# Kernel optimization log

Measured on AMD Instinct MI355X. Metric: run time of the kernel, lower is better.

Reference implementation:

```python
import jax, jax.numpy as jnp
import numpy as np

TEXT_DIM = 1024
FEAT_DIM = 1024
NUM_HEADS = 16
HEAD_DIM = FEAT_DIM // NUM_HEADS
EPS = 1e-6


def rms_norm(x, w):
    # LlamaRMSNorm: compute in fp32, scale by learned weight
    xf = x.astype(jnp.float32)
    var = jnp.mean(xf * xf, axis=-1, keepdims=True)
    return (xf * jax.lax.rsqrt(var + EPS)).astype(x.dtype) * w


def setup_inputs() -> dict:
    key = jax.random.key(0)
    ks = jax.random.split(key, 8)
    def xavier(k, shape, gain=1.0):
        fan_in, fan_out = shape[1], shape[0]
        lim = gain * np.sqrt(6.0 / (fan_in + fan_out))
        return jax.random.uniform(k, shape, jnp.float32, -lim, lim)
    return {
        "text": jax.random.normal(ks[0], (8, 512, TEXT_DIM), jnp.float32),
        "features": jax.random.normal(ks[1], (8, 1024, FEAT_DIM), jnp.float32),
        "W_q": xavier(ks[2], (FEAT_DIM, TEXT_DIM)),
        "b_q": jnp.zeros((FEAT_DIM,), jnp.float32),
        "W_k": xavier(ks[3], (FEAT_DIM, FEAT_DIM)),
        "b_k": jnp.zeros((FEAT_DIM,), jnp.float32),
        "W_o": xavier(ks[4], (FEAT_DIM, FEAT_DIM), gain=0.1),
        "b_o": jnp.zeros((FEAT_DIM,), jnp.float32),
        "g_feat": jnp.ones((FEAT_DIM,), jnp.float32),
        "g_q": jnp.ones((FEAT_DIM,), jnp.float32),
        "g_k": jnp.ones((FEAT_DIM,), jnp.float32),
    }


def reference(text, features, W_q, b_q, W_k, b_k, W_o, b_o, g_feat, g_q, g_k):
    B, T, _ = text.shape
    _, N, _ = features.shape
    feats = rms_norm(features, g_feat)                      # [B,N,Df]
    Q = rms_norm(text @ W_q.T + b_q, g_q)                   # [B,T,Df]
    K = rms_norm(feats @ W_k.T + b_k, g_k)                  # [B,N,Df]
    Qh = Q.reshape(B, T, NUM_HEADS, HEAD_DIM)
    Kh = K.reshape(B, N, NUM_HEADS, HEAD_DIM)
    Vh = feats.reshape(B, N, NUM_HEADS, HEAD_DIM)
    scores = jnp.einsum("bthd,bnhd->bhtn", Qh, Kh) / np.sqrt(HEAD_DIM).astype(np.float32)
    attn = jax.nn.softmax(scores, axis=-1)                  # [B,H,T,N]
    out = jnp.einsum("bhtn,bnhd->bthd", attn, Vh).reshape(B, T, FEAT_DIM)
    return out @ W_o.T + b_o
```

## Files before the change

### kernel.cpp

```cpp
#include <hip/hip_runtime.h>
#include <hip/hip_bf16.h>


typedef unsigned short u16;
typedef __bf16 bf16x8 __attribute__((ext_vector_type(8)));
typedef float f32x4 __attribute__((ext_vector_type(4)));

__device__ inline f32x4 mfma16(bf16x8 a, bf16x8 b, f32x4 c) {
    return __builtin_amdgcn_mfma_f32_16x16x32_bf16(a, b, c, 0, 0, 0);
}

__device__ inline u16 f2bf(float f) {
    union { float f; unsigned u; } v; v.f = f;
    unsigned r = v.u + 0x7fffu + ((v.u >> 16) & 1u);
    return (u16)(r >> 16);
}

__device__ inline float bf2f(u16 x) {
    union { unsigned u; float f; } v; v.u = ((unsigned)x) << 16; return v.f;
}

__device__ inline unsigned pk_bf16(float a, float b) {
    union { float f; unsigned u; } x, y; x.f = a; y.f = b;
    return __builtin_amdgcn_perm(y.u + 0x8000u, x.u + 0x8000u, 0x07060302u);
}

__device__ inline void load_lds16(const void* g, void* l) {
    __builtin_amdgcn_global_load_lds(
        (const __attribute__((address_space(1))) void*)g,
        (__attribute__((address_space(3))) void*)l, 16, 0, 0);
}

__global__ __launch_bounds__(256) void cast_rows_kernel(const float* __restrict__ text,
                                                        const float* __restrict__ Wq,
                                                        const float* __restrict__ Wk,
                                                        const float* __restrict__ Wo,
                                                        const float* __restrict__ features,
                                                        u16* __restrict__ otext, u16* __restrict__ oWq,
                                                        u16* __restrict__ oWk, u16* __restrict__ oWo,
                                                        float* __restrict__ ssbuf) {
    int blk = blockIdx.x, tid = threadIdx.x;
    if (blk < 7168) {
        int i = blk * 256 + tid;
        const float* src; u16* dst; int off;
        if (i < 1048576)      { src = text; dst = otext; off = i; }
        else if (i < 1310720) { src = Wq;   dst = oWq;   off = i - 1048576; }
        else if (i < 1572864) { src = Wk;   dst = oWk;   off = i - 1310720; }
        else                  { src = Wo;   dst = oWo;   off = i - 1572864; }
        float4 v = ((const float4*)src)[off];
        uint2 p; p.x = pk_bf16(v.x, v.y); p.y = pk_bf16(v.z, v.w);
        ((uint2*)dst)[off] = p;
    } else {
        int row = (blk - 7168) * 4 + (tid >> 6);
        int lane = tid & 63;
        const float4* rp = (const float4*)(features + (size_t)row * 1024) + lane * 4;
        float ss = 0.0f;
        #pragma unroll
        for (int i = 0; i < 4; ++i) {
            float4 v = rp[i];
            ss += v.x * v.x + v.y * v.y + v.z * v.z + v.w * v.w;
        }
        #pragma unroll
        for (int m = 1; m < 64; m <<= 1) ss += __shfl_xor(ss, m, 64);
        if (lane == 0) ssbuf[row] = ss;
    }
}

__global__ __launch_bounds__(256) void normT_kernel(const float* __restrict__ features,
                                                    const float* __restrict__ ssbuf,
                                                    const float* __restrict__ g,
                                                    u16* __restrict__ feats_bf,
                                                    u16* __restrict__ Vt) {
    __shared__ __align__(16) u16 tile[64][72];
    int tid = threadIdx.x, b = blockIdx.z;
    int n0 = blockIdx.x * 64, d0 = blockIdx.y * 64;
    int r = tid >> 2, cs = (tid & 3) * 16;
    int grow = b * 1024 + n0 + r;

    float rs = rsqrtf(ssbuf[grow] * (1.0f / 1024.0f) + 1e-6f);
    const float4* src = (const float4*)(features + (size_t)grow * 1024 + d0 + cs);
    const float4* gp  = (const float4*)(g + d0 + cs);
    union { u16 s[16]; uint4 v[2]; } ob;
    #pragma unroll
    for (int i = 0; i < 4; ++i) {
        float4 v = src[i], gv = gp[i];
        unsigned lo = pk_bf16(v.x * rs * gv.x, v.y * rs * gv.y);
        unsigned hi = pk_bf16(v.z * rs * gv.z, v.w * rs * gv.w);
        ((unsigned*)ob.s)[i * 2]     = lo;
        ((unsigned*)ob.s)[i * 2 + 1] = hi;
    }
    uint4* dst = (uint4*)(feats_bf + (size_t)grow * 1024 + d0 + cs);
    dst[0] = ob.v[0]; dst[1] = ob.v[1];
    #pragma unroll
    for (int i = 0; i < 16; ++i) tile[r][cs + i] = ob.s[i];
    __syncthreads();
    union { u16 s[8]; uint4 v; } t0, t1;
    #pragma unroll
    for (int i = 0; i < 8; ++i) { t0.s[i] = tile[cs + i][r]; t1.s[i] = tile[cs + 8 + i][r]; }
    u16* tdst = Vt + ((size_t)(b * 1024 + d0 + r)) * 1024 + n0 + cs;
    *(uint4*)tdst = t0.v;
    *(uint4*)(tdst + 8) = t1.v;
}

__global__ __launch_bounds__(256) void rmsnorm_qk_kernel(u16* __restrict__ QK,
                                                         const float* __restrict__ g_q,
                                                         const float* __restrict__ g_k,
                                                         float qscale) {
    int tid = threadIdx.x;
    int row = blockIdx.x * 4 + (tid >> 6);
    int lane = tid & 63;
    const float* g = (row < 4096) ? g_q : g_k;
    float outsc = (row < 4096) ? qscale : 1.0f;

    u16* rp = QK + (size_t)row * 1024 + lane * 16;
    union { u16 s[16]; uint4 v[2]; } in;
    in.v[0] = *(const uint4*)rp;
    in.v[1] = *(const uint4*)(rp + 8);
    float x[16], ss = 0.0f;
    #pragma unroll
    for (int i = 0; i < 16; ++i) { x[i] = bf2f(in.s[i]); ss += x[i] * x[i]; }
    #pragma unroll
    for (int m = 1; m < 64; m <<= 1) ss += __shfl_xor(ss, m, 64);
    float rs = rsqrtf(ss * (1.0f / 1024.0f) + 1e-6f) * outsc;
    const float4* gp = (const float4*)(g + lane * 16);
    union { unsigned u[8]; uint4 v[2]; } ob;
    #pragma unroll
    for (int i = 0; i < 4; ++i) {
        float4 gv = gp[i];
        ob.u[i * 2]     = pk_bf16(x[i * 4 + 0] * rs * gv.x, x[i * 4 + 1] * rs * gv.y);
        ob.u[i * 2 + 1] = pk_bf16(x[i * 4 + 2] * rs * gv.z, x[i * 4 + 3] * rs * gv.w);
    }
    *(uint4*)rp = ob.v[0];
    *(uint4*)(rp + 8) = ob.v[1];
}

template <bool BF16OUT>
__device__ __forceinline__ void gemm64_bk64(const u16* __restrict__ A, const u16* __restrict__ B,
                                            const float* __restrict__ bias, void* __restrict__ Cout,
                                            int m_blk, int n_blk, int K, int N,
                                            u16* As, u16* Bs) {
    int tid = threadIdx.x, wave = tid >> 6, lane = tid & 63;
    int quad = lane >> 4, l15 = lane & 15;
    int wm = wave & 1, wn = wave >> 1;
    int srl = lane >> 3, scl = lane & 7;
    const int swz = (scl ^ srl) * 8;

    f32x4 acc[4][2] = {};

    auto stage = [&](int buf, int k0) {
        u16* Ad = As + buf * (128 * 64);
        u16* Bd = Bs + buf * (64 * 64);
        #pragma unroll
        for (int is = 0; is < 4; ++is) {
            int row = is * 32 + wave * 8 + srl;
            load_lds16(A + (size_t)(m_blk + row) * K + k0 + swz,
                       Ad + (is * 32 + wave * 8) * 64);
        }
        #pragma unroll
        for (int is = 0; is < 2; ++is) {
            int row = is * 32 + wave * 8 + srl;
            load_lds16(B + (size_t)(n_blk + row) * K + k0 + swz,
                       Bd + (is * 32 + wave * 8) * 64);
        }
    };

    stage(0, 0);
    __syncthreads();
    int cur = 0;

    for (int k0 = 0; k0 < K; k0 += 64) {
        if (k0 + 64 < K) stage(cur ^ 1, k0 + 64);

        const u16* Ar = As + cur * (128 * 64);
        const u16* Br = Bs + cur * (64 * 64);
        #pragma unroll
        for (int kh = 0; kh < 2; ++kh) {
            bf16x8 af[4], bfr[2];
            int co = ((kh * 4 + quad) ^ (l15 & 7)) * 8;
            #pragma unroll
            for (int t = 0; t < 4; ++t)
                af[t] = *(const bf16x8*)&Ar[(wm * 64 + t * 16 + l15) * 64 + co];
            #pragma unroll
            for (int t = 0; t < 2; ++t)
                bfr[t] = *(const bf16x8*)&Br[(wn * 32 + t * 16 + l15) * 64 + co];
            #pragma unroll
            for (int mt = 0; mt < 4; ++mt)
                #pragma unroll
                for (int nt = 0; nt < 2; ++nt)
                    acc[mt][nt] = mfma16(af[mt], bfr[nt], acc[mt][nt]);
        }
        __syncthreads();
        cur ^= 1;
    }

    #pragma unroll
    for (int nt = 0; nt < 2; ++nt) {
        int col = n_blk + wn * 32 + nt * 16 + l15;
        float bv = bias[col];
        #pragma unroll
        for (int mt = 0; mt < 4; ++mt) {
            int row0 = m_blk + wm * 64 + mt * 16 + quad * 4;
            #pragma unroll
            for (int r = 0; r < 4; ++r) {
                float val = acc[mt][nt][r] + bv;
                if (BF16OUT) ((u16*)Cout)[(size_t)(row0 + r) * N + col] = f2bf(val);
                else       ((float*)Cout)[(size_t)(row0 + r) * N + col] = val;
            }
        }
    }
}

__global__ __launch_bounds__(256) void gemm_qk_kernel(const u16* __restrict__ text_bf,
                                                      const u16* __restrict__ Wq,
                                                      const u16* __restrict__ feats_bf,
                                                      const u16* __restrict__ Wk,
                                                      const float* __restrict__ b_q,
                                                      const float* __restrict__ b_k,
                                                      u16* __restrict__ QK) {
    __shared__ __align__(16) u16 As[2 * 128 * 64];
    __shared__ __align__(16) u16 Bs[2 * 64 * 64];
    int id = blockIdx.x;
    if (id < 512) {
        gemm64_bk64<true>(text_bf, Wq, b_q, QK, (id & 31) * 128, (id >> 5) * 64, 1024, 1024, As, Bs);
    } else {
        id -= 512;
        gemm64_bk64<true>(feats_bf, Wk, b_k, QK + 4096 * 1024,
                          (id & 63) * 128, (id >> 6) * 64, 1024, 1024, As, Bs);
    }
}

__global__ __launch_bounds__(256) void gemm_o_kernel(const u16* __restrict__ A,
                                                     const u16* __restrict__ B,
                                                     const float* __restrict__ bias,
                                                     float* __restrict__ C) {
    __shared__ __align__(16) u16 As[2 * 128 * 64];
    __shared__ __align__(16) u16 Bs[2 * 64 * 64];
    int id = blockIdx.x;
    gemm64_bk64<false>(A, B, bias, C, (id & 31) * 128, (id >> 5) * 64, 1024, 1024, As, Bs);
}

__global__ __launch_bounds__(256) void attn_kernel(const u16* __restrict__ Q,
                                                   const u16* __restrict__ K,
                                                   const u16* __restrict__ Vt,
                                                   u16* __restrict__ Out) {
    int bh = blockIdx.x, qt = blockIdx.y;
    int b = bh >> 4, h = bh & 15;
    int tid = threadIdx.x, wave = tid >> 6, lane = tid & 63;
    int quad = lane >> 4, l15 = lane & 15;

    __shared__ __align__(16) u16 Ks[2][64 * 64];
    __shared__ __align__(16) u16 Vs[2][64 * 64];
    __shared__ __align__(16) u16 Plds[4][16 * 64];
    u16* Pw = &Plds[wave][0];
    const int psw = (l15 & 7) << 3;

    const size_t qoff = ((size_t)(b * 512 + qt * 64 + wave * 16 + l15)) * 1024 + h * 64 + quad * 8;
    bf16x8 qf0 = *(const bf16x8*)(Q + qoff);
    bf16x8 qf1 = *(const bf16x8*)(Q + qoff + 32);

    int srl = lane >> 3, scl = lane & 7;
    const u16* Kbase = K + ((size_t)(b * 1024)) * 1024 + h * 64;
    const u16* Vbase = Vt + ((size_t)(b * 1024 + h * 64)) * 1024;

    __bf16 onev = (__bf16)1.0f;
    bf16x8 ones = {onev, onev, onev, onev, onev, onev, onev, onev};

    f32x4 o[4] = {};
    f32x4 lac = {0.0f, 0.0f, 0.0f, 0.0f};

    auto stage = [&](int buf, int n0) {
        #pragma unroll
        for (int j = 0; j < 2; ++j) {
            int row = wave * 16 + j * 8 + srl;
            load_lds16(Kbase + (size_t)(n0 + row) * 1024 + (scl ^ srl) * 8,
                       &Ks[buf][(wave * 16 + j * 8) * 64]);
            load_lds16(Vbase + (size_t)row * 1024 + n0 + (scl ^ srl) * 8,
                       &Vs[buf][(wave * 16 + j * 8) * 64]);
        }
    };

    stage(0, 0);
    __syncthreads();
    int cur = 0;

    for (int n0 = 0; n0 < 1024; n0 += 64) {
        if (n0 < 960) stage(cur ^ 1, n0 + 64);

        f32x4 s[4];
        __builtin_amdgcn_s_setprio(1);
        #pragma unroll
        for (int nt = 0; nt < 4; ++nt) {
            int R = nt * 16 + l15;
            int c1 = (quad ^ (l15 & 7)) * 8;
            bf16x8 kf0 = *(const bf16x8*)&Ks[cur][R * 64 + c1];
            bf16x8 kf1 = *(const bf16x8*)&Ks[cur][R * 64 + (c1 ^ 32)];
            f32x4 z = {-16.0f, -16.0f, -16.0f, -16.0f};
            s[nt] = mfma16(kf0, qf0, z);
            s[nt] = mfma16(kf1, qf1, s[nt]);
        }
        __builtin_amdgcn_s_setprio(0);

        #pragma unroll
        for (int nt = 0; nt < 4; ++nt) {
            uint2 pk;
            pk.x = pk_bf16(exp2f(s[nt][0]), exp2f(s[nt][1]));
            pk.y = pk_bf16(exp2f(s[nt][2]), exp2f(s[nt][3]));
            *(uint2*)&Pw[l15 * 64 + ((nt * 16 + quad * 4) ^ psw)] = pk;
        }

        bf16x8 pf[2];
        #pragma unroll
        for (int kc = 0; kc < 2; ++kc)
            pf[kc] = *(const bf16x8*)&Pw[l15 * 64 + ((kc * 32 + quad * 8) ^ psw)];
        __builtin_amdgcn_s_setprio(1);
        #pragma unroll
        for (int kc = 0; kc < 2; ++kc) {
            lac = mfma16(ones, pf[kc], lac);
            #pragma unroll
            for (int dt = 0; dt < 4; ++dt) {
                int d = dt * 16 + l15;
                int ch = ((kc * 4 + quad) ^ (l15 & 7)) * 8;
                bf16x8 vf = *(const bf16x8*)&Vs[cur][d * 64 + ch];
                o[dt] = mfma16(vf, pf[kc], o[dt]);
            }
        }
        __builtin_amdgcn_s_setprio(0);

        __syncthreads();
        cur ^= 1;
    }

    float il = 1.0f / lac[0];
    size_t obase = ((size_t)(b * 512 + qt * 64 + wave * 16 + l15)) * 1024 + h * 64 + quad * 4;
    #pragma unroll
    for (int dt = 0; dt < 4; ++dt) {
        uint2 pk;
        pk.x = pk_bf16(o[dt][0] * il, o[dt][1] * il);
        pk.y = pk_bf16(o[dt][2] * il, o[dt][3] * il);
        *(uint2*)(Out + obase + dt * 16) = pk;
    }
}

extern "C" void kernel_launch(void* const* d_in, const int* in_sizes, int n_in,
                              void* d_out, int out_size, void* d_ws, size_t ws_size,
                              hipStream_t stream) {
    const float* text     = (const float*)d_in[0];
    const float* features = (const float*)d_in[1];
    const float* W_q      = (const float*)d_in[2];
    const float* b_q      = (const float*)d_in[3];
    const float* W_k      = (const float*)d_in[4];
    const float* b_k      = (const float*)d_in[5];
    const float* W_o      = (const float*)d_in[6];
    const float* b_o      = (const float*)d_in[7];
    const float* g_feat   = (const float*)d_in[8];
    const float* g_q      = (const float*)d_in[9];
    const float* g_k      = (const float*)d_in[10];

    char* ws = (char*)d_ws;
    u16*   text_bf  = (u16*)(ws + 0);
    u16*   Wq_bf    = (u16*)(ws + 8388608);
    u16*   Wk_bf    = (u16*)(ws + 10485760);
    u16*   Wo_bf    = (u16*)(ws + 12582912);
    u16*   feats_bf = (u16*)(ws + 14680064);
    u16*   Vt       = (u16*)(ws + 31457280);
    u16*   QKbuf    = (u16*)(ws + 48234496);
    u16*   attn_bf  = (u16*)(ws + 73400320);
    float* ssbuf    = (float*)(ws + 81788928);

    const float QSCALE = 0.18033688011112042f;

    cast_rows_kernel<<<9216, 256, 0, stream>>>(text, W_q, W_k, W_o, features,
                                               text_bf, Wq_bf, Wk_bf, Wo_bf, ssbuf);
    normT_kernel<<<dim3(16, 16, 8), 256, 0, stream>>>(features, ssbuf, g_feat, feats_bf, Vt);
    gemm_qk_kernel<<<1536, 256, 0, stream>>>(text_bf, Wq_bf, feats_bf, Wk_bf, b_q, b_k, QKbuf);
    rmsnorm_qk_kernel<<<3072, 256, 0, stream>>>(QKbuf, g_q, g_k, QSCALE);
    attn_kernel<<<dim3(128, 8), 256, 0, stream>>>(QKbuf, QKbuf + 4096 * 1024, Vt, attn_bf);
    gemm_o_kernel<<<512, 256, 0, stream>>>(attn_bf, Wo_bf, b_o, (float*)d_out);
}
```

Before: 225.2 us.

## Split attention waves 2x2 over query and key tiles with LDS reduction

Reorganizes the attention kernel so each wave handles 32 query rows and half of each 64-key tile, instead of 16 query rows and the full tile. This reuses each loaded K and V fragment across two query subtiles, cutting LDS reads per MFMA. Partial outputs and softmax denominators from the two key halves are combined through LDS at the end. It also switches to native exp2 and adds an occupancy hint, at the cost of more registers per thread and an extra reduction step.

```diff
diff --git a/kernel.cpp b/kernel.cpp
--- a/kernel.cpp
+++ b/kernel.cpp
@@ -5,6 +5,8 @@
 typedef unsigned short u16;
 typedef __bf16 bf16x8 __attribute__((ext_vector_type(8)));
 typedef float f32x4 __attribute__((ext_vector_type(4)));
+
+extern "C" __device__ float __ocml_native_exp2_f32(float);
 
 __device__ inline f32x4 mfma16(bf16x8 a, bf16x8 b, f32x4 c) {
     return __builtin_amdgcn_mfma_f32_16x16x32_bf16(a, b, c, 0, 0, 0);
@@ -239,24 +241,30 @@
     gemm64_bk64<false>(A, B, bias, C, (id & 31) * 128, (id >> 5) * 64, 1024, 1024, As, Bs);
 }
 
-__global__ __launch_bounds__(256) void attn_kernel(const u16* __restrict__ Q,
-                                                   const u16* __restrict__ K,
-                                                   const u16* __restrict__ Vt,
-                                                   u16* __restrict__ Out) {
+__global__ __launch_bounds__(256, 4) void attn_kernel(const u16* __restrict__ Q,
+                                                      const u16* __restrict__ K,
+                                                      const u16* __restrict__ Vt,
+                                                      u16* __restrict__ Out) {
     int bh = blockIdx.x, qt = blockIdx.y;
     int b = bh >> 4, h = bh & 15;
     int tid = threadIdx.x, wave = tid >> 6, lane = tid & 63;
     int quad = lane >> 4, l15 = lane & 15;
+    int wq = wave & 1, wn = wave >> 1;
 
     __shared__ __align__(16) u16 Ks[2][64 * 64];
     __shared__ __align__(16) u16 Vs[2][64 * 64];
-    __shared__ __align__(16) u16 Plds[4][16 * 64];
+    __shared__ __align__(16) u16 Plds[4][2 * 16 * 32];
     u16* Pw = &Plds[wave][0];
-    const int psw = (l15 & 7) << 3;
-
-    const size_t qoff = ((size_t)(b * 512 + qt * 64 + wave * 16 + l15)) * 1024 + h * 64 + quad * 8;
-    bf16x8 qf0 = *(const bf16x8*)(Q + qoff);
-    bf16x8 qf1 = *(const bf16x8*)(Q + qoff + 32);
+    const int pfs = (l15 >> 1) & 3;
+
+    bf16x8 qf[2][2];
+    #pragma unroll
+    for (int mt = 0; mt < 2; ++mt) {
+        const size_t qoff =
+            ((size_t)(b * 512 + qt * 64 + wq * 32 + mt * 16 + l15)) * 1024 + h * 64 + quad * 8;
+        qf[mt][0] = *(const bf16x8*)(Q + qoff);
+        qf[mt][1] = *(const bf16x8*)(Q + qoff + 32);
+    }
 
     int srl = lane >> 3, scl = lane & 7;
     const u16* Kbase = K + ((size_t)(b * 1024)) * 1024 + h * 64;
@@ -265,8 +273,8 @@
     __bf16 onev = (__bf16)1.0f;
     bf16x8 ones = {onev, onev, onev, onev, onev, onev, onev, onev};
 
-    f32x4 o[4] = {};
-    f32x4 lac = {0.0f, 0.0f, 0.0f, 0.0f};
+    f32x4 o[2][4] = {};
+    f32x4 lac[2] = {{0.0f, 0.0f, 0.0f, 0.0f}, {0.0f, 0.0f, 0.0f, 0.0f}};
 
     auto stage = [&](int buf, int n0) {
         #pragma unroll
@@ -286,43 +294,51 @@
     for (int n0 = 0; n0 < 1024; n0 += 64) {
         if (n0 < 960) stage(cur ^ 1, n0 + 64);
 
-        f32x4 s[4];
+        f32x4 s[2][2];
         __builtin_amdgcn_s_setprio(1);
         #pragma unroll
-        for (int nt = 0; nt < 4; ++nt) {
-            int R = nt * 16 + l15;
+        for (int nt = 0; nt < 2; ++nt) {
+            int R = wn * 32 + nt * 16 + l15;
             int c1 = (quad ^ (l15 & 7)) * 8;
             bf16x8 kf0 = *(const bf16x8*)&Ks[cur][R * 64 + c1];
             bf16x8 kf1 = *(const bf16x8*)&Ks[cur][R * 64 + (c1 ^ 32)];
-            f32x4 z = {-16.0f, -16.0f, -16.0f, -16.0f};
-            s[nt] = mfma16(kf0, qf0, z);
-            s[nt] = mfma16(kf1, qf1, s[nt]);
+            #pragma unroll
+            for (int mt = 0; mt < 2; ++mt) {
+                f32x4 z = {-16.0f, -16.0f, -16.0f, -16.0f};
+                s[mt][nt] = mfma16(kf0, qf[mt][0], z);
+                s[mt][nt] = mfma16(kf1, qf[mt][1], s[mt][nt]);
+            }
         }
         __builtin_amdgcn_s_setprio(0);
 
         #pragma unroll
-        for (int nt = 0; nt < 4; ++nt) {
-            uint2 pk;
-            pk.x = pk_bf16(exp2f(s[nt][0]), exp2f(s[nt][1]));
-            pk.y = pk_bf16(exp2f(s[nt][2]), exp2f(s[nt][3]));
-            *(uint2*)&Pw[l15 * 64 + ((nt * 16 + quad * 4) ^ psw)] = pk;
-        }
-
-        bf16x8 pf[2];
-        #pragma unroll
-        for (int kc = 0; kc < 2; ++kc)
-            pf[kc] = *(const bf16x8*)&Pw[l15 * 64 + ((kc * 32 + quad * 8) ^ psw)];
+        for (int mt = 0; mt < 2; ++mt)
+            #pragma unroll
+            for (int nt = 0; nt < 2; ++nt) {
+                uint2 pk;
+                pk.x = pk_bf16(__ocml_native_exp2_f32(s[mt][nt][0]),
+                               __ocml_native_exp2_f32(s[mt][nt][1]));
+                pk.y = pk_bf16(__ocml_native_exp2_f32(s[mt][nt][2]),
+                               __ocml_native_exp2_f32(s[mt][nt][3]));
+                *(uint2*)&Pw[mt * 512 + l15 * 32 + (((nt * 4 + quad) ^ (pfs << 1)) << 2)] = pk;
+            }
+
+        bf16x8 pf[2], vf[4];
+        #pragma unroll
+        for (int mt = 0; mt < 2; ++mt)
+            pf[mt] = *(const bf16x8*)&Pw[mt * 512 + l15 * 32 + ((quad ^ pfs) << 3)];
+        #pragma unroll
+        for (int dt = 0; dt < 4; ++dt) {
+            int ch = ((wn * 4 + quad) ^ (l15 & 7)) * 8;
+            vf[dt] = *(const bf16x8*)&Vs[cur][(dt * 16 + l15) * 64 + ch];
+        }
         __builtin_amdgcn_s_setprio(1);
         #pragma unroll
-        for (int kc = 0; kc < 2; ++kc) {
-            lac = mfma16(ones, pf[kc], lac);
-            #pragma unroll
-            for (int dt = 0; dt < 4; ++dt) {
-                int d = dt * 16 + l15;
-                int ch = ((kc * 4 + quad) ^ (l15 & 7)) * 8;
-                bf16x8 vf = *(const bf16x8*)&Vs[cur][d * 64 + ch];
-                o[dt] = mfma16(vf, pf[kc], o[dt]);
-            }
+        for (int mt = 0; mt < 2; ++mt) {
+            lac[mt] = mfma16(ones, pf[mt], lac[mt]);
+            #pragma unroll
+            for (int dt = 0; dt < 4; ++dt)
+                o[mt][dt] = mfma16(vf[dt], pf[mt], o[mt][dt]);
         }
         __builtin_amdgcn_s_setprio(0);
 
@@ -330,14 +346,36 @@
         cur ^= 1;
     }
 
-    float il = 1.0f / lac[0];
-    size_t obase = ((size_t)(b * 512 + qt * 64 + wave * 16 + l15)) * 1024 + h * 64 + quad * 4;
-    #pragma unroll
-    for (int dt = 0; dt < 4; ++dt) {
-        uint2 pk;
-        pk.x = pk_bf16(o[dt][0] * il, o[dt][1] * il);
-        pk.y = pk_bf16(o[dt][2] * il, o[dt][3] * il);
-        *(uint2*)(Out + obase + dt * 16) = pk;
+    float* Ored = (float*)&Ks[0][0];
+    float* Lred = (float*)&Vs[0][0];
+    if (wn == 1) {
+        #pragma unroll
+        for (int mt = 0; mt < 2; ++mt) {
+            #pragma unroll
+            for (int dt = 0; dt < 4; ++dt) {
+                int c = mt * 4 + dt;
+                *(f32x4*)&Ored[wq * 2048 + lane * 32 + ((c ^ (lane & 7)) << 2)] = o[mt][dt];
+            }
+            Lred[wq * 128 + lane * 2 + mt] = lac[mt][0];
+        }
+    }
+    __syncthreads();
+    if (wn == 0) {
+        #pragma unroll
+        for (int mt = 0; mt < 2; ++mt) {
+            float il = 1.0f / (lac[mt][0] + Lred[wq * 128 + lane * 2 + mt]);
+            size_t obase =
+                ((size_t)(b * 512 + qt * 64 + wq * 32 + mt * 16 + l15)) * 1024 + h * 64 + quad * 4;
+            #pragma unroll
+            for (int dt = 0; dt < 4; ++dt) {
+                int c = mt * 4 + dt;
+                f32x4 oo = o[mt][dt] + *(const f32x4*)&Ored[wq * 2048 + lane * 32 + ((c ^ (lane & 7)) << 2)];
+                uint2 pk;
+                pk.x = pk_bf16(oo[0] * il, oo[1] * il);
+                pk.y = pk_bf16(oo[2] * il, oo[3] * il);
+                *(uint2*)(Out + obase + dt * 16) = pk;
+            }
+        }
     }
 }
 
```

After: 218.2 us. -3.1%, faster.
